# Kernel tuning notes

Hardware: AMD Instinct MI355X
Metric: run time of the kernel (lower is better)

## Reference

```python
import jax, jax.numpy as jnp
import numpy as np

NEG_INF = -1e30


def setup_inputs() -> dict:
    key = jax.random.key(0)
    kq, kk, kv, ks = jax.random.split(key, 4)
    B, H, S, D = 2, 16, 2048, 64
    return {
        "q": jax.random.normal(kq, (B, H, S, D), dtype=jnp.float32),
        "k": jax.random.normal(kk, (B, H, S, D), dtype=jnp.float32),
        "v": jax.random.normal(kv, (B, H, S, D), dtype=jnp.float32),
        "sink_weights": jax.random.normal(ks, (H,), dtype=jnp.float32),
        "sliding_window": 1024,
    }


def reference(q, k, v, sink_weights, sliding_window):
    """Sliding-window causal attention with a learnable attention-sink logit.

    Equivalent to FlexAttention.forward with sink_weights given: an extra kv
    position (the sink) is appended whose score is replaced by sink_weights[h]
    and whose value is zero -> it only adds mass to the softmax denominator.
    """
    B, H, S_q, D = q.shape
    S_kv = k.shape[2]
    scale = 1.0 / np.sqrt(D)

    # [B, H, S_q, S_kv] raw scores
    scores = jnp.einsum("bhqd,bhkd->bhqk", q, k) * scale

    q_idx = jnp.arange(S_q)[:, None]
    kv_idx = jnp.arange(S_kv)[None, :]
    keep = (kv_idx <= q_idx) & (q_idx - kv_idx <= sliding_window)  # [S_q, S_kv]
    scores = jnp.where(keep[None, None], scores, NEG_INF)

    # sink column: per-head learnable logit, always visible
    sink_col = jnp.broadcast_to(
        sink_weights[None, :, None, None], (B, H, S_q, 1)
    )
    logits = jnp.concatenate([scores, sink_col], axis=-1)  # [B,H,S_q,S_kv+1]

    probs = jax.nn.softmax(logits, axis=-1)
    # sink value is zero, so only the first S_kv prob columns hit v
    out = jnp.einsum("bhqk,bhkd->bhqd", probs[..., :S_kv], v)
    return out
```

## Files before the change

kernel.cpp:

```cpp
#include <hip/hip_runtime.h>


typedef __bf16 bf16x8 __attribute__((ext_vector_type(8)));
typedef __bf16 bf16x4 __attribute__((ext_vector_type(4)));
typedef float  f32x16 __attribute__((ext_vector_type(16)));

#define NT 256
#define NEG_BIG (-3.0e38f)

__device__ __forceinline__ int swz(int row, int gran) {
    return row * 64 + ((gran ^ ((row >> 1) & 7)) << 3);
}

__device__ __forceinline__ bf16x4 xswap32(bf16x4 v) {
    union { bf16x4 v; int i[2]; } u;
    u.v = v;
    u.i[0] = __shfl_xor(u.i[0], 32, 64);
    u.i[1] = __shfl_xor(u.i[1], 32, 64);
    return u.v;
}

__device__ const int SEG_N[24] = {3,2,2,2,2,1,2,1, 1,1,1,1,1,1,1,1, 1,1,1,1,1,1,1,1};
__device__ const int SEG_IT[24][3] = {
  {0,1,2},{2,3,0},{3,4,0},{4,5,0},{5,6,0},{6,0,0},{6,7,0},{7,0,0},
  {8,0,0},{8,0,0},{9,0,0},{9,0,0},{10,0,0},{10,0,0},{11,0,0},{11,0,0},
  {12,0,0},{12,0,0},{13,0,0},{13,0,0},{14,0,0},{14,0,0},{15,0,0},{15,0,0}};
__device__ const int SEG_J0[24][3] = {
  {0,0,0},{3,0,0},{6,0,0},{7,0,0},{6,0,0},{3,0,0},{12,0,0},{7,0,0},
  {0,0,0},{9,0,0},{0,0,0},{9,0,0},{0,0,0},{9,0,0},{0,0,0},{9,0,0},
  {0,0,0},{9,0,0},{0,0,0},{9,0,0},{0,0,0},{9,0,0},{0,0,0},{9,0,0}};
__device__ const int SEG_J1[24][3] = {
  {2,4,3},{6,6,0},{8,7,0},{10,6,0},{12,3,0},{12,0,0},{14,7,0},{16,0,0},
  {9,0,0},{18,0,0},{9,0,0},{18,0,0},{9,0,0},{18,0,0},{9,0,0},{18,0,0},
  {9,0,0},{18,0,0},{9,0,0},{18,0,0},{9,0,0},{18,0,0},{9,0,0},{18,0,0}};
__device__ const int SEG_SX[24][3] = {
  {0,0,0},{1,0,0},{1,0,0},{1,0,0},{1,0,0},{1,0,0},{2,0,0},{1,0,0},
  {0,0,0},{1,0,0},{0,0,0},{1,0,0},{0,0,0},{1,0,0},{0,0,0},{1,0,0},
  {0,0,0},{1,0,0},{0,0,0},{1,0,0},{0,0,0},{1,0,0},{0,0,0},{1,0,0}};
__device__ const int NSEG_ITEM[16] = {1,1,2,2,2,2,3,2, 2,2,2,2,2,2,2,2};

__device__ __forceinline__ void qk_mfma(const __bf16* kb, const bf16x8 bq[4],
                                        int c, int hl, f32x16& s0, f32x16& s1) {
    #pragma unroll
    for (int ks = 0; ks < 4; ++ks) {
        bf16x8 ka0 = *(const bf16x8*)&kb[swz(c,      2 * ks + hl)];
        bf16x8 ka1 = *(const bf16x8*)&kb[swz(32 + c, 2 * ks + hl)];
        s0 = __builtin_amdgcn_mfma_f32_32x32x16_bf16(ka0, bq[ks], s0, 0, 0, 0);
        s1 = __builtin_amdgcn_mfma_f32_32x32x16_bf16(ka1, bq[ks], s1, 0, 0, 0);
    }
}

__device__ __forceinline__ void pv_mfma(const __bf16* vb, const bf16x8 bp[4],
                                        int c, int hl, f32x16& o0, f32x16& o1) {
    #pragma unroll
    for (int ks = 0; ks < 4; ++ks) {
        bf16x8 va0 = *(const bf16x8*)&vb[swz(c,      2 * ks + hl)];
        bf16x8 va1 = *(const bf16x8*)&vb[swz(32 + c, 2 * ks + hl)];
        o0 = __builtin_amdgcn_mfma_f32_32x32x16_bf16(va0, bp[ks], o0, 0, 0, 0);
        o1 = __builtin_amdgcn_mfma_f32_32x32x16_bf16(va1, bp[ks], o1, 0, 0, 0);
    }
}

__device__ __forceinline__ void mask_tile(f32x16& s0, f32x16& s1,
                                          int k0, int qi, int W, int hl) {
    #pragma unroll
    for (int rg = 0; rg < 16; ++rg) {
        const int kb2 = (rg & 3) + 8 * (rg >> 2) + 4 * hl;
        const int ki0 = k0 + kb2, ki1 = k0 + 32 + kb2;
        if (!((ki0 <= qi) && (qi - ki0 <= W))) s0[rg] = -1e30f;
        if (!((ki1 <= qi) && (qi - ki1 <= W))) s1[rg] = -1e30f;
    }
}

__device__ __forceinline__ void exch_bp(const f32x16 s0, const f32x16 s1,
                                        int hl, bf16x8 bp[4]) {
    bf16x4 qA = { (__bf16)s0[0],  (__bf16)s0[1],  (__bf16)s0[2],  (__bf16)s0[3]  };
    bf16x4 qB = { (__bf16)s0[4],  (__bf16)s0[5],  (__bf16)s0[6],  (__bf16)s0[7]  };
    bf16x4 qC = { (__bf16)s0[8],  (__bf16)s0[9],  (__bf16)s0[10], (__bf16)s0[11] };
    bf16x4 qD = { (__bf16)s0[12], (__bf16)s0[13], (__bf16)s0[14], (__bf16)s0[15] };
    bf16x4 qE = { (__bf16)s1[0],  (__bf16)s1[1],  (__bf16)s1[2],  (__bf16)s1[3]  };
    bf16x4 qF = { (__bf16)s1[4],  (__bf16)s1[5],  (__bf16)s1[6],  (__bf16)s1[7]  };
    bf16x4 qG = { (__bf16)s1[8],  (__bf16)s1[9],  (__bf16)s1[10], (__bf16)s1[11] };
    bf16x4 qH = { (__bf16)s1[12], (__bf16)s1[13], (__bf16)s1[14], (__bf16)s1[15] };
    bf16x4 r0 = xswap32(hl ? qA : qB);
    bf16x4 r1 = xswap32(hl ? qC : qD);
    bf16x4 r2 = xswap32(hl ? qE : qF);
    bf16x4 r3 = xswap32(hl ? qG : qH);
    bf16x4 lo0 = hl ? r0 : qA, hi0 = hl ? qB : r0;
    bf16x4 lo1 = hl ? r1 : qC, hi1 = hl ? qD : r1;
    bf16x4 lo2 = hl ? r2 : qE, hi2 = hl ? qF : r2;
    bf16x4 lo3 = hl ? r3 : qG, hi3 = hl ? qH : r3;
    #pragma unroll
    for (int e = 0; e < 4; ++e) {
        bp[0][e] = lo0[e]; bp[0][4+e] = hi0[e];
        bp[1][e] = lo1[e]; bp[1][4+e] = hi1[e];
        bp[2][e] = lo2[e]; bp[2][4+e] = hi2[e];
        bp[3][e] = lo3[e]; bp[3][4+e] = hi3[e];
    }
}

__device__ __forceinline__ void stage_k(__bf16* dst, const float4* kr, int t) {
    #pragma unroll
    for (int i = 0; i < 4; ++i) {
        const int flat = i * NT + t;
        const int key = flat >> 4, dd = flat & 15;
        float4 f = kr[i];
        bf16x4 b = { (__bf16)f.x, (__bf16)f.y, (__bf16)f.z, (__bf16)f.w };
        *(bf16x4*)&dst[swz(key, dd >> 1) + (dd & 1) * 4] = b;
    }
}

__device__ __forceinline__ void stage_v(__bf16* dst, const float4* vr, int dgi, int kgi) {
    float4 a0 = vr[0], a1 = vr[1], a2 = vr[2], a3 = vr[3];
    bf16x4 w0 = { (__bf16)a0.x, (__bf16)a1.x, (__bf16)a2.x, (__bf16)a3.x };
    bf16x4 w1 = { (__bf16)a0.y, (__bf16)a1.y, (__bf16)a2.y, (__bf16)a3.y };
    bf16x4 w2 = { (__bf16)a0.z, (__bf16)a1.z, (__bf16)a2.z, (__bf16)a3.z };
    bf16x4 w3 = { (__bf16)a0.w, (__bf16)a1.w, (__bf16)a2.w, (__bf16)a3.w };
    const int gv = kgi >> 1, ov = (kgi & 1) * 4;
    *(bf16x4*)&dst[swz(4 * dgi + 0, gv) + ov] = w0;
    *(bf16x4*)&dst[swz(4 * dgi + 1, gv) + ov] = w1;
    *(bf16x4*)&dst[swz(4 * dgi + 2, gv) + ov] = w2;
    *(bf16x4*)&dst[swz(4 * dgi + 3, gv) + ov] = w3;
}

__global__ __launch_bounds__(NT, 2) void flex_r14_main(
    const float* __restrict__ Q, const float* __restrict__ K,
    const float* __restrict__ V, const float* __restrict__ SINKW,
    const int* __restrict__ SWIN, void* __restrict__ WS,
    float* __restrict__ OUT, const int H, const int S)
{
    const int t    = threadIdx.x;
    const int lane = t & 63;
    const int w    = t >> 6;
    const int c    = lane & 31;
    const int hl   = lane >> 5;
    const int W    = SWIN[0];
    const float scale = 0.125f;

    const int NBH = gridDim.x / 24;
    int bh, b24;
    if ((NBH & 7) == 0) {
        const int xcd  = blockIdx.x & 7;
        const int rest = blockIdx.x >> 3;
        const int G    = NBH >> 3;
        bh  = (rest % G) * 8 + xcd;
        b24 = rest / G;
    } else {
        bh  = blockIdx.x / 24;
        b24 = blockIdx.x - bh * 24;
    }
    const int h   = bh % H;
    const float sw = SINKW[h];

    __shared__ __align__(16) __bf16 k_lds[2][2][64 * 64];
    __shared__ __align__(16) __bf16 v_lds[2][2][64 * 64];

    const size_t basebh = (size_t)bh * S * 64;
    const float4* kp4 = (const float4*)(K + basebh);
    const float4* vp4 = (const float4*)(V + basebh);
    __bf16* O_ws  = (__bf16*)WS;
    float2* ml_ws = (float2*)((char*)WS + (size_t)NBH * 48 * 16384);

    const int dgi = t & 15;
    const int kgi = t >> 4;
    float4 kreg[8], vreg[8];

    const int ns = SEG_N[b24];

    {
        const int it0 = SEG_IT[b24][0];
        const int ktA0 = (2 * it0 - 16 > 0) ? (2 * it0 - 16) : 0;
        const int kt0 = ktA0 + SEG_J0[b24][0];
        #pragma unroll
        for (int i = 0; i < 4; ++i) {
            kreg[i]     = kp4[kt0 * 1024 + i * NT + t];
            kreg[4 + i] = kp4[(kt0 + 1) * 1024 + i * NT + t];
        }
        #pragma unroll
        for (int kk = 0; kk < 4; ++kk) {
            vreg[kk]     = vp4[kt0 * 1024 + (4 * kgi + kk) * 16 + dgi];
            vreg[4 + kk] = vp4[(kt0 + 1) * 1024 + (4 * kgi + kk) * 16 + dgi];
        }
        stage_k(&k_lds[0][0][0], &kreg[0], t);
        stage_v(&v_lds[0][0][0], &vreg[0], dgi, kgi);
        stage_k(&k_lds[0][1][0], &kreg[4], t);
        stage_v(&v_lds[0][1][0], &vreg[4], dgi, kgi);
    }

    int par = 0;

    for (int s = 0; s < ns; ++s) {
        const int item = SEG_IT[b24][s];
        const int j0   = SEG_J0[b24][s];
        const int j1   = SEG_J1[b24][s];
        const int sidx = SEG_SX[b24][s];
        const int ktA  = (2 * item - 16 > 0) ? (2 * item - 16) : 0;
        const int qw0  = item * 128 + 32 * w;
        const int qi   = qw0 + c;

        bf16x8 bq[4];
        {
            const float4* qp4 = (const float4*)(Q + basebh + (size_t)qi * 64);
            #pragma unroll
            for (int ks = 0; ks < 4; ++ks) {
                float4 f0 = qp4[4 * ks + 2 * hl];
                float4 f1 = qp4[4 * ks + 2 * hl + 1];
                bq[ks][0] = (__bf16)(f0.x * scale); bq[ks][1] = (__bf16)(f0.y * scale);
                bq[ks][2] = (__bf16)(f0.z * scale); bq[ks][3] = (__bf16)(f0.w * scale);
                bq[ks][4] = (__bf16)(f1.x * scale); bq[ks][5] = (__bf16)(f1.y * scale);
                bq[ks][6] = (__bf16)(f1.z * scale); bq[ks][7] = (__bf16)(f1.w * scale);
            }
        }

        float mrun = (sidx == 0) ? sw : NEG_BIG;
        float lrun = (sidx == 0) ? 1.0f : 0.0f;
        f32x16 accO0, accO1;
        #pragma unroll
        for (int i = 0; i < 16; ++i) { accO0[i] = 0.0f; accO1[i] = 0.0f; }

        for (int j = j0; j < j1; j += 2) {
            const bool two = (j + 1 < j1);
            const int k0a = (ktA + j) * 64;
            const int k0b = k0a + 64;

            __syncthreads();

            int n0 = -1, n1 = -1;
            if (j + 2 < j1) {
                n0 = ktA + j + 2;
                if (j + 3 < j1) n1 = n0 + 1;
            } else if (s + 1 < ns) {
                const int it2  = SEG_IT[b24][s + 1];
                const int ktA2 = (2 * it2 - 16 > 0) ? (2 * it2 - 16) : 0;
                const int j02  = SEG_J0[b24][s + 1];
                n0 = ktA2 + j02;
                if (j02 + 1 < SEG_J1[b24][s + 1]) n1 = n0 + 1;
            }
            if (n0 >= 0) {
                #pragma unroll
                for (int i = 0; i < 4; ++i) kreg[i] = kp4[n0 * 1024 + i * NT + t];
                #pragma unroll
                for (int kk = 0; kk < 4; ++kk) vreg[kk] = vp4[n0 * 1024 + (4 * kgi + kk) * 16 + dgi];
            }
            if (n1 >= 0) {
                #pragma unroll
                for (int i = 0; i < 4; ++i) kreg[4 + i] = kp4[n1 * 1024 + i * NT + t];
                #pragma unroll
                for (int kk = 0; kk < 4; ++kk) vreg[4 + kk] = vp4[n1 * 1024 + (4 * kgi + kk) * 16 + dgi];
            }

            f32x16 sa0, sa1, sb0, sb1;
            #pragma unroll
            for (int i = 0; i < 16; ++i) { sa0[i] = 0.0f; sa1[i] = 0.0f; sb0[i] = 0.0f; sb1[i] = 0.0f; }
            __builtin_amdgcn_s_setprio(1);
            qk_mfma(&k_lds[par][0][0], bq, c, hl, sa0, sa1);
            if (two) qk_mfma(&k_lds[par][1][0], bq, c, hl, sb0, sb1);
            __builtin_amdgcn_s_setprio(0);

            if (!((k0a + 63 <= qw0) && (qw0 + 31 - k0a <= W)))
                mask_tile(sa0, sa1, k0a, qi, W, hl);
            if (two && !((k0b + 63 <= qw0) && (qw0 + 31 - k0b <= W)))
                mask_tile(sb0, sb1, k0b, qi, W, hl);

            float m8[8];
            #pragma unroll
            for (int i = 0; i < 4; ++i) {
                m8[i]   = fmaxf(fmaxf(sa0[4*i], sa0[4*i+1]), fmaxf(sa0[4*i+2], sa0[4*i+3]));
                m8[4+i] = fmaxf(fmaxf(sa1[4*i], sa1[4*i+1]), fmaxf(sa1[4*i+2], sa1[4*i+3]));
            }
            float mx = fmaxf(fmaxf(fmaxf(m8[0], m8[1]), fmaxf(m8[2], m8[3])),
                             fmaxf(fmaxf(m8[4], m8[5]), fmaxf(m8[6], m8[7])));
            if (two) {
                float n8[8];
                #pragma unroll
                for (int i = 0; i < 4; ++i) {
                    n8[i]   = fmaxf(fmaxf(sb0[4*i], sb0[4*i+1]), fmaxf(sb0[4*i+2], sb0[4*i+3]));
                    n8[4+i] = fmaxf(fmaxf(sb1[4*i], sb1[4*i+1]), fmaxf(sb1[4*i+2], sb1[4*i+3]));
                }
                mx = fmaxf(mx, fmaxf(fmaxf(fmaxf(n8[0], n8[1]), fmaxf(n8[2], n8[3])),
                                     fmaxf(fmaxf(n8[4], n8[5]), fmaxf(n8[6], n8[7]))));
            }
            mx = fmaxf(mx, __shfl_xor(mx, 32, 64));
            if (!__all(mx <= mrun + 8.0f)) {
                const float mnew  = fmaxf(mrun, mx);
                const float alpha = __expf(mrun - mnew);
                lrun *= alpha;
                #pragma unroll
                for (int i = 0; i < 16; ++i) { accO0[i] *= alpha; accO1[i] *= alpha; }
                mrun = mnew;
            }
            float sc[8];
            #pragma unroll
            for (int i = 0; i < 8; ++i) sc[i] = 0.0f;
            #pragma unroll
            for (int i = 0; i < 16; ++i) {
                float p0 = __expf(sa0[i] - mrun); sa0[i] = p0; sc[i & 3]       += p0;
                float p1 = __expf(sa1[i] - mrun); sa1[i] = p1; sc[4 + (i & 3)] += p1;
            }
            if (two) {
                #pragma unroll
                for (int i = 0; i < 16; ++i) {
                    float p0 = __expf(sb0[i] - mrun); sb0[i] = p0; sc[i & 3]       += p0;
                    float p1 = __expf(sb1[i] - mrun); sb1[i] = p1; sc[4 + (i & 3)] += p1;
                }
            }
            float ps = ((sc[0] + sc[1]) + (sc[2] + sc[3])) + ((sc[4] + sc[5]) + (sc[6] + sc[7]));
            ps += __shfl_xor(ps, 32, 64);
            lrun += ps;

            {
                bf16x8 bp[4];
                exch_bp(sa0, sa1, hl, bp);
                __builtin_amdgcn_s_setprio(1);
                pv_mfma(&v_lds[par][0][0], bp, c, hl, accO0, accO1);
                __builtin_amdgcn_s_setprio(0);
            }
            if (two) {
                bf16x8 bp[4];
                exch_bp(sb0, sb1, hl, bp);
                __builtin_amdgcn_s_setprio(1);
                pv_mfma(&v_lds[par][1][0], bp, c, hl, accO0, accO1);
                __builtin_amdgcn_s_setprio(0);
            }

            if (n0 >= 0) {
                stage_k(&k_lds[par ^ 1][0][0], &kreg[0], t);
                stage_v(&v_lds[par ^ 1][0][0], &vreg[0], dgi, kgi);
            }
            if (n1 >= 0) {
                stage_k(&k_lds[par ^ 1][1][0], &kreg[4], t);
                stage_v(&v_lds[par ^ 1][1][0], &vreg[4], dgi, kgi);
            }
            par ^= 1;
        }

        if (item < 2) {
            const float inv = 1.0f / lrun;
            float* ob = OUT + basebh + (size_t)qi * 64;
            #pragma unroll
            for (int rg = 0; rg < 4; ++rg) {
                float4 f0 = { accO0[4*rg+0]*inv, accO0[4*rg+1]*inv,
                              accO0[4*rg+2]*inv, accO0[4*rg+3]*inv };
                float4 f1 = { accO1[4*rg+0]*inv, accO1[4*rg+1]*inv,
                              accO1[4*rg+2]*inv, accO1[4*rg+3]*inv };
                *(float4*)&ob[     8 * rg + 4 * hl] = f0;
                *(float4*)&ob[32 + 8 * rg + 4 * hl] = f1;
            }
        } else {
            const int slot = (bh * 16 + item) * 3 + sidx;
            const int qrel = 32 * w + c;
            if (hl == 0) ml_ws[(size_t)slot * 128 + qrel] = make_float2(mrun, lrun);
            __bf16* Os = O_ws + (size_t)slot * 8192 + (size_t)qrel * 64;
            #pragma unroll
            for (int qd = 0; qd < 4; ++qd) {
                const int d0 = 8 * qd + 4 * hl;
                bf16x4 b0 = { (__bf16)accO0[4*qd+0], (__bf16)accO0[4*qd+1],
                              (__bf16)accO0[4*qd+2], (__bf16)accO0[4*qd+3] };
                bf16x4 b1 = { (__bf16)accO1[4*qd+0], (__bf16)accO1[4*qd+1],
                              (__bf16)accO1[4*qd+2], (__bf16)accO1[4*qd+3] };
                *(bf16x4*)&Os[d0]      = b0;
                *(bf16x4*)&Os[32 + d0] = b1;
            }
        }
    }
}

__global__ __launch_bounds__(256) void flex_r14_combine(
    const void* __restrict__ WS, float* __restrict__ OUT, const int H, const int S)
{
    const int NBH  = gridDim.x / 14;
    const int bi   = blockIdx.x;
    const int bh   = bi / 14;
    const int item = 2 + (bi - bh * 14);
    const int ns   = NSEG_ITEM[item];
    const int t    = threadIdx.x;
    const int q    = t >> 1;
    const int half = t & 1;

    const __bf16* O_ws = (const __bf16*)WS;
    const float2* ml_ws = (const float2*)((const char*)WS + (size_t)NBH * 48 * 16384);
    const int base = (bh * 16 + item) * 3;

    float m[3], lv[3], a[3];
    float mst = NEG_BIG;
    for (int s = 0; s < ns; ++s) {
        float2 e = ml_ws[(size_t)(base + s) * 128 + q];
        m[s] = e.x; lv[s] = e.y;
        mst = fmaxf(mst, m[s]);
    }
    float lst = 0.0f;
    for (int s = 0; s < ns; ++s) { a[s] = __expf(m[s] - mst); lst += a[s] * lv[s]; }
    const float inv = 1.0f / lst;

    float acc[32];
    #pragma unroll
    for (int i = 0; i < 32; ++i) acc[i] = 0.0f;
    for (int s = 0; s < ns; ++s) {
        const __bf16* Os = O_ws + (size_t)(base + s) * 8192 + (size_t)q * 64 + 32 * half;
        const float as = a[s];
        #pragma unroll
        for (int v8 = 0; v8 < 4; ++v8) {
            bf16x8 o = *(const bf16x8*)&Os[8 * v8];
            #pragma unroll
            for (int jj = 0; jj < 8; ++jj) acc[8 * v8 + jj] += as * (float)o[jj];
        }
    }

    float* dst = OUT + (size_t)bh * S * 64 + (size_t)(item * 128 + q) * 64 + 32 * half;
    #pragma unroll
    for (int v4 = 0; v4 < 8; ++v4) {
        float4 f = { acc[4*v4+0] * inv, acc[4*v4+1] * inv,
                     acc[4*v4+2] * inv, acc[4*v4+3] * inv };
        *(float4*)&dst[4 * v4] = f;
    }
}

extern "C" void kernel_launch(void* const* d_in, const int* in_sizes, int n_in,
                              void* d_out, int out_size, void* d_ws, size_t ws_size,
                              hipStream_t stream) {
    const float* q     = (const float*)d_in[0];
    const float* k     = (const float*)d_in[1];
    const float* v     = (const float*)d_in[2];
    const float* sinkw = (const float*)d_in[3];
    const int*   swin  = (const int*)d_in[4];
    float* out = (float*)d_out;

    const int H = in_sizes[3];
    const int S = 2048;
    const int B = in_sizes[0] / (H * S * 64);
    const int NBH = B * H;

    flex_r14_main<<<dim3(NBH * 24), NT, 0, stream>>>(q, k, v, sinkw, swin, d_ws, out, H, S);
    flex_r14_combine<<<dim3(NBH * 14), 256, 0, stream>>>(d_ws, out, H, S);
}
```

Baseline: 143.5 us.

## Single-buffer K/V LDS, raise occupancy to 3, use permlane32 swaps

Replaces the double-buffered K/V shared-memory tiles with a single buffer, so each iteration stages from registers into LDS between two barriers. The prefetch global loads now move to after the softmax and before the PV MFMAs. Launch bounds rise from 2 to 3 blocks per CU, which the halved LDS footprint allows. Cross-half lane exchanges (max, sum, P operand reshuffle) switch from shfl_xor to v_permlane32_swap, dropping the hl-dependent selects. The trade-off is an extra barrier per iteration and less overlap between staging and compute, in exchange for more resident waves and cheaper exchanges.

```diff
diff --git a/kernel.cpp b/kernel.cpp
--- a/kernel.cpp
+++ b/kernel.cpp
@@ -12,12 +12,115 @@
     return row * 64 + ((gran ^ ((row >> 1) & 7)) << 3);
 }
 
-__device__ __forceinline__ bf16x4 xswap32(bf16x4 v) {
-    union { bf16x4 v; int i[2]; } u;
-    u.v = v;
-    u.i[0] = __shfl_xor(u.i[0], 32, 64);
-    u.i[1] = __shfl_xor(u.i[1], 32, 64);
-    return u.v;
+__device__ __forceinline__ void plswap(unsigned &a, unsigned &b) {
+    asm("v_permlane32_swap_b32 %0, %1" : "+v"(a), "+v"(b));
+}
+
+__device__ __forceinline__ float xmax32(float x) {
+    float a = x, b;
+    asm("v_mov_b32 %0, %1" : "=&v"(b) : "v"(a));
+    asm("v_permlane32_swap_b32 %0, %1" : "+v"(a), "+v"(b));
+    return fmaxf(a, b);
+}
+
+__device__ __forceinline__ float xsum32(float x) {
+    float a = x, b;
+    asm("v_mov_b32 %0, %1" : "=&v"(b) : "v"(a));
+    asm("v_permlane32_swap_b32 %0, %1" : "+v"(a), "+v"(b));
+    return a + b;
+}
+
+__device__ __forceinline__ void exch_bp(const f32x16& sa, const f32x16& sb,
+                                        bf16x8 bp[4]) {
+    union B4U { bf16x4 v; unsigned u[2]; };
+    B4U a0, b0, a1, b1, a2, b2, a3, b3;
+    a0.v = bf16x4{ (__bf16)sa[0],  (__bf16)sa[1],  (__bf16)sa[2],  (__bf16)sa[3]  };
+    b0.v = bf16x4{ (__bf16)sa[4],  (__bf16)sa[5],  (__bf16)sa[6],  (__bf16)sa[7]  };
+    a1.v = bf16x4{ (__bf16)sa[8],  (__bf16)sa[9],  (__bf16)sa[10], (__bf16)sa[11] };
+    b1.v = bf16x4{ (__bf16)sa[12], (__bf16)sa[13], (__bf16)sa[14], (__bf16)sa[15] };
+    a2.v = bf16x4{ (__bf16)sb[0],  (__bf16)sb[1],  (__bf16)sb[2],  (__bf16)sb[3]  };
+    b2.v = bf16x4{ (__bf16)sb[4],  (__bf16)sb[5],  (__bf16)sb[6],  (__bf16)sb[7]  };
+    a3.v = bf16x4{ (__bf16)sb[8],  (__bf16)sb[9],  (__bf16)sb[10], (__bf16)sb[11] };
+    b3.v = bf16x4{ (__bf16)sb[12], (__bf16)sb[13], (__bf16)sb[14], (__bf16)sb[15] };
+    plswap(a0.u[0], b0.u[0]); plswap(a0.u[1], b0.u[1]);
+    plswap(a1.u[0], b1.u[0]); plswap(a1.u[1], b1.u[1]);
+    plswap(a2.u[0], b2.u[0]); plswap(a2.u[1], b2.u[1]);
+    plswap(a3.u[0], b3.u[0]); plswap(a3.u[1], b3.u[1]);
+    #pragma unroll
+    for (int e = 0; e < 4; ++e) {
+        bp[0][e] = a0.v[e]; bp[0][4+e] = b0.v[e];
+        bp[1][e] = a1.v[e]; bp[1][4+e] = b1.v[e];
+        bp[2][e] = a2.v[e]; bp[2][4+e] = b2.v[e];
+        bp[3][e] = a3.v[e]; bp[3][4+e] = b3.v[e];
+    }
+}
+
+__device__ __forceinline__ void mask_tile(f32x16& s0, f32x16& s1,
+                                          int k0, int qi, int W, int hl) {
+    #pragma unroll
+    for (int rg = 0; rg < 16; ++rg) {
+        const int kb2 = (rg & 3) + 8 * (rg >> 2) + 4 * hl;
+        const int ki0 = k0 + kb2, ki1 = k0 + 32 + kb2;
+        if (!((ki0 <= qi) && (qi - ki0 <= W))) s0[rg] = -1e30f;
+        if (!((ki1 <= qi) && (qi - ki1 <= W))) s1[rg] = -1e30f;
+    }
+}
+
+__device__ __forceinline__ float tree_max(const f32x16& s0, const f32x16& s1) {
+    float q4[8];
+    #pragma unroll
+    for (int i = 0; i < 4; ++i) {
+        q4[i]   = fmaxf(fmaxf(s0[4*i], s0[4*i+1]), fmaxf(s0[4*i+2], s0[4*i+3]));
+        q4[4+i] = fmaxf(fmaxf(s1[4*i], s1[4*i+1]), fmaxf(s1[4*i+2], s1[4*i+3]));
+    }
+    return fmaxf(fmaxf(fmaxf(q4[0], q4[1]), fmaxf(q4[2], q4[3])),
+                 fmaxf(fmaxf(q4[4], q4[5]), fmaxf(q4[6], q4[7])));
+}
+
+__device__ __forceinline__ void qk_mfma(const __bf16* kb, const bf16x8 bq[4],
+                                        int c, int hl, f32x16& s0, f32x16& s1) {
+    #pragma unroll
+    for (int ks = 0; ks < 4; ++ks) {
+        bf16x8 ka0 = *(const bf16x8*)&kb[swz(c,      2 * ks + hl)];
+        bf16x8 ka1 = *(const bf16x8*)&kb[swz(32 + c, 2 * ks + hl)];
+        s0 = __builtin_amdgcn_mfma_f32_32x32x16_bf16(ka0, bq[ks], s0, 0, 0, 0);
+        s1 = __builtin_amdgcn_mfma_f32_32x32x16_bf16(ka1, bq[ks], s1, 0, 0, 0);
+    }
+}
+
+__device__ __forceinline__ void pv_mfma(const __bf16* vb, const bf16x8 bp[4],
+                                        int c, int hl, f32x16& o0, f32x16& o1) {
+    #pragma unroll
+    for (int ks = 0; ks < 4; ++ks) {
+        bf16x8 va0 = *(const bf16x8*)&vb[swz(c,      2 * ks + hl)];
+        bf16x8 va1 = *(const bf16x8*)&vb[swz(32 + c, 2 * ks + hl)];
+        o0 = __builtin_amdgcn_mfma_f32_32x32x16_bf16(va0, bp[ks], o0, 0, 0, 0);
+        o1 = __builtin_amdgcn_mfma_f32_32x32x16_bf16(va1, bp[ks], o1, 0, 0, 0);
+    }
+}
+
+__device__ __forceinline__ void stage_k(__bf16* dst, const float4* kr, int t) {
+    #pragma unroll
+    for (int i = 0; i < 4; ++i) {
+        const int flat = i * NT + t;
+        const int key = flat >> 4, dd = flat & 15;
+        float4 f = kr[i];
+        bf16x4 b = { (__bf16)f.x, (__bf16)f.y, (__bf16)f.z, (__bf16)f.w };
+        *(bf16x4*)&dst[swz(key, dd >> 1) + (dd & 1) * 4] = b;
+    }
+}
+
+__device__ __forceinline__ void stage_v(__bf16* dst, const float4* vr, int dgi, int kgi) {
+    float4 a0 = vr[0], a1 = vr[1], a2 = vr[2], a3 = vr[3];
+    bf16x4 w0 = { (__bf16)a0.x, (__bf16)a1.x, (__bf16)a2.x, (__bf16)a3.x };
+    bf16x4 w1 = { (__bf16)a0.y, (__bf16)a1.y, (__bf16)a2.y, (__bf16)a3.y };
+    bf16x4 w2 = { (__bf16)a0.z, (__bf16)a1.z, (__bf16)a2.z, (__bf16)a3.z };
+    bf16x4 w3 = { (__bf16)a0.w, (__bf16)a1.w, (__bf16)a2.w, (__bf16)a3.w };
+    const int gv = kgi >> 1, ov = (kgi & 1) * 4;
+    *(bf16x4*)&dst[swz(4 * dgi + 0, gv) + ov] = w0;
+    *(bf16x4*)&dst[swz(4 * dgi + 1, gv) + ov] = w1;
+    *(bf16x4*)&dst[swz(4 * dgi + 2, gv) + ov] = w2;
+    *(bf16x4*)&dst[swz(4 * dgi + 3, gv) + ov] = w3;
 }
 
 __device__ const int SEG_N[24] = {3,2,2,2,2,1,2,1, 1,1,1,1,1,1,1,1, 1,1,1,1,1,1,1,1};
@@ -39,91 +142,7 @@
   {0,0,0},{1,0,0},{0,0,0},{1,0,0},{0,0,0},{1,0,0},{0,0,0},{1,0,0}};
 __device__ const int NSEG_ITEM[16] = {1,1,2,2,2,2,3,2, 2,2,2,2,2,2,2,2};
 
-__device__ __forceinline__ void qk_mfma(const __bf16* kb, const bf16x8 bq[4],
-                                        int c, int hl, f32x16& s0, f32x16& s1) {
-    #pragma unroll
-    for (int ks = 0; ks < 4; ++ks) {
-        bf16x8 ka0 = *(const bf16x8*)&kb[swz(c,      2 * ks + hl)];
-        bf16x8 ka1 = *(const bf16x8*)&kb[swz(32 + c, 2 * ks + hl)];
-        s0 = __builtin_amdgcn_mfma_f32_32x32x16_bf16(ka0, bq[ks], s0, 0, 0, 0);
-        s1 = __builtin_amdgcn_mfma_f32_32x32x16_bf16(ka1, bq[ks], s1, 0, 0, 0);
-    }
-}
-
-__device__ __forceinline__ void pv_mfma(const __bf16* vb, const bf16x8 bp[4],
-                                        int c, int hl, f32x16& o0, f32x16& o1) {
-    #pragma unroll
-    for (int ks = 0; ks < 4; ++ks) {
-        bf16x8 va0 = *(const bf16x8*)&vb[swz(c,      2 * ks + hl)];
-        bf16x8 va1 = *(const bf16x8*)&vb[swz(32 + c, 2 * ks + hl)];
-        o0 = __builtin_amdgcn_mfma_f32_32x32x16_bf16(va0, bp[ks], o0, 0, 0, 0);
-        o1 = __builtin_amdgcn_mfma_f32_32x32x16_bf16(va1, bp[ks], o1, 0, 0, 0);
-    }
-}
-
-__device__ __forceinline__ void mask_tile(f32x16& s0, f32x16& s1,
-                                          int k0, int qi, int W, int hl) {
-    #pragma unroll
-    for (int rg = 0; rg < 16; ++rg) {
-        const int kb2 = (rg & 3) + 8 * (rg >> 2) + 4 * hl;
-        const int ki0 = k0 + kb2, ki1 = k0 + 32 + kb2;
-        if (!((ki0 <= qi) && (qi - ki0 <= W))) s0[rg] = -1e30f;
-        if (!((ki1 <= qi) && (qi - ki1 <= W))) s1[rg] = -1e30f;
-    }
-}
-
-__device__ __forceinline__ void exch_bp(const f32x16 s0, const f32x16 s1,
-                                        int hl, bf16x8 bp[4]) {
-    bf16x4 qA = { (__bf16)s0[0],  (__bf16)s0[1],  (__bf16)s0[2],  (__bf16)s0[3]  };
-    bf16x4 qB = { (__bf16)s0[4],  (__bf16)s0[5],  (__bf16)s0[6],  (__bf16)s0[7]  };
-    bf16x4 qC = { (__bf16)s0[8],  (__bf16)s0[9],  (__bf16)s0[10], (__bf16)s0[11] };
-    bf16x4 qD = { (__bf16)s0[12], (__bf16)s0[13], (__bf16)s0[14], (__bf16)s0[15] };
-    bf16x4 qE = { (__bf16)s1[0],  (__bf16)s1[1],  (__bf16)s1[2],  (__bf16)s1[3]  };
-    bf16x4 qF = { (__bf16)s1[4],  (__bf16)s1[5],  (__bf16)s1[6],  (__bf16)s1[7]  };
-    bf16x4 qG = { (__bf16)s1[8],  (__bf16)s1[9],  (__bf16)s1[10], (__bf16)s1[11] };
-    bf16x4 qH = { (__bf16)s1[12], (__bf16)s1[13], (__bf16)s1[14], (__bf16)s1[15] };
-    bf16x4 r0 = xswap32(hl ? qA : qB);
-    bf16x4 r1 = xswap32(hl ? qC : qD);
-    bf16x4 r2 = xswap32(hl ? qE : qF);
-    bf16x4 r3 = xswap32(hl ? qG : qH);
-    bf16x4 lo0 = hl ? r0 : qA, hi0 = hl ? qB : r0;
-    bf16x4 lo1 = hl ? r1 : qC, hi1 = hl ? qD : r1;
-    bf16x4 lo2 = hl ? r2 : qE, hi2 = hl ? qF : r2;
-    bf16x4 lo3 = hl ? r3 : qG, hi3 = hl ? qH : r3;
-    #pragma unroll
-    for (int e = 0; e < 4; ++e) {
-        bp[0][e] = lo0[e]; bp[0][4+e] = hi0[e];
-        bp[1][e] = lo1[e]; bp[1][4+e] = hi1[e];
-        bp[2][e] = lo2[e]; bp[2][4+e] = hi2[e];
-        bp[3][e] = lo3[e]; bp[3][4+e] = hi3[e];
-    }
-}
-
-__device__ __forceinline__ void stage_k(__bf16* dst, const float4* kr, int t) {
-    #pragma unroll
-    for (int i = 0; i < 4; ++i) {
-        const int flat = i * NT + t;
-        const int key = flat >> 4, dd = flat & 15;
-        float4 f = kr[i];
-        bf16x4 b = { (__bf16)f.x, (__bf16)f.y, (__bf16)f.z, (__bf16)f.w };
-        *(bf16x4*)&dst[swz(key, dd >> 1) + (dd & 1) * 4] = b;
-    }
-}
-
-__device__ __forceinline__ void stage_v(__bf16* dst, const float4* vr, int dgi, int kgi) {
-    float4 a0 = vr[0], a1 = vr[1], a2 = vr[2], a3 = vr[3];
-    bf16x4 w0 = { (__bf16)a0.x, (__bf16)a1.x, (__bf16)a2.x, (__bf16)a3.x };
-    bf16x4 w1 = { (__bf16)a0.y, (__bf16)a1.y, (__bf16)a2.y, (__bf16)a3.y };
-    bf16x4 w2 = { (__bf16)a0.z, (__bf16)a1.z, (__bf16)a2.z, (__bf16)a3.z };
-    bf16x4 w3 = { (__bf16)a0.w, (__bf16)a1.w, (__bf16)a2.w, (__bf16)a3.w };
-    const int gv = kgi >> 1, ov = (kgi & 1) * 4;
-    *(bf16x4*)&dst[swz(4 * dgi + 0, gv) + ov] = w0;
-    *(bf16x4*)&dst[swz(4 * dgi + 1, gv) + ov] = w1;
-    *(bf16x4*)&dst[swz(4 * dgi + 2, gv) + ov] = w2;
-    *(bf16x4*)&dst[swz(4 * dgi + 3, gv) + ov] = w3;
-}
-
-__global__ __launch_bounds__(NT, 2) void flex_r14_main(
+__global__ __launch_bounds__(NT, 3) void flex_r19_main(
     const float* __restrict__ Q, const float* __restrict__ K,
     const float* __restrict__ V, const float* __restrict__ SINKW,
     const int* __restrict__ SWIN, void* __restrict__ WS,
@@ -152,8 +171,8 @@
     const int h   = bh % H;
     const float sw = SINKW[h];
 
-    __shared__ __align__(16) __bf16 k_lds[2][2][64 * 64];
-    __shared__ __align__(16) __bf16 v_lds[2][2][64 * 64];
+    __shared__ __align__(16) __bf16 k_lds[2][64 * 64];
+    __shared__ __align__(16) __bf16 v_lds[2][64 * 64];
 
     const size_t basebh = (size_t)bh * S * 64;
     const float4* kp4 = (const float4*)(K + basebh);
@@ -181,13 +200,7 @@
             vreg[kk]     = vp4[kt0 * 1024 + (4 * kgi + kk) * 16 + dgi];
             vreg[4 + kk] = vp4[(kt0 + 1) * 1024 + (4 * kgi + kk) * 16 + dgi];
         }
-        stage_k(&k_lds[0][0][0], &kreg[0], t);
-        stage_v(&v_lds[0][0][0], &vreg[0], dgi, kgi);
-        stage_k(&k_lds[0][1][0], &kreg[4], t);
-        stage_v(&v_lds[0][1][0], &vreg[4], dgi, kgi);
-    }
-
-    int par = 0;
+    }
 
     for (int s = 0; s < ns; ++s) {
         const int item = SEG_IT[b24][s];
@@ -222,6 +235,15 @@
             const bool two = (j + 1 < j1);
             const int k0a = (ktA + j) * 64;
             const int k0b = k0a + 64;
+
+            __syncthreads();
+
+            stage_k(&k_lds[0][0], &kreg[0], t);
+            stage_v(&v_lds[0][0], &vreg[0], dgi, kgi);
+            if (two) {
+                stage_k(&k_lds[1][0], &kreg[4], t);
+                stage_v(&v_lds[1][0], &vreg[4], dgi, kgi);
+            }
 
             __syncthreads();
 
@@ -236,25 +258,13 @@
                 n0 = ktA2 + j02;
                 if (j02 + 1 < SEG_J1[b24][s + 1]) n1 = n0 + 1;
             }
-            if (n0 >= 0) {
-                #pragma unroll
-                for (int i = 0; i < 4; ++i) kreg[i] = kp4[n0 * 1024 + i * NT + t];
-                #pragma unroll
-                for (int kk = 0; kk < 4; ++kk) vreg[kk] = vp4[n0 * 1024 + (4 * kgi + kk) * 16 + dgi];
-            }
-            if (n1 >= 0) {
-                #pragma unroll
-                for (int i = 0; i < 4; ++i) kreg[4 + i] = kp4[n1 * 1024 + i * NT + t];
-                #pragma unroll
-                for (int kk = 0; kk < 4; ++kk) vreg[4 + kk] = vp4[n1 * 1024 + (4 * kgi + kk) * 16 + dgi];
-            }
 
             f32x16 sa0, sa1, sb0, sb1;
             #pragma unroll
             for (int i = 0; i < 16; ++i) { sa0[i] = 0.0f; sa1[i] = 0.0f; sb0[i] = 0.0f; sb1[i] = 0.0f; }
             __builtin_amdgcn_s_setprio(1);
-            qk_mfma(&k_lds[par][0][0], bq, c, hl, sa0, sa1);
-            if (two) qk_mfma(&k_lds[par][1][0], bq, c, hl, sb0, sb1);
+            qk_mfma(&k_lds[0][0], bq, c, hl, sa0, sa1);
+            if (two) qk_mfma(&k_lds[1][0], bq, c, hl, sb0, sb1);
             __builtin_amdgcn_s_setprio(0);
 
             if (!((k0a + 63 <= qw0) && (qw0 + 31 - k0a <= W)))
@@ -262,25 +272,9 @@
             if (two && !((k0b + 63 <= qw0) && (qw0 + 31 - k0b <= W)))
                 mask_tile(sb0, sb1, k0b, qi, W, hl);
 
-            float m8[8];
-            #pragma unroll
-            for (int i = 0; i < 4; ++i) {
-                m8[i]   = fmaxf(fmaxf(sa0[4*i], sa0[4*i+1]), fmaxf(sa0[4*i+2], sa0[4*i+3]));
-                m8[4+i] = fmaxf(fmaxf(sa1[4*i], sa1[4*i+1]), fmaxf(sa1[4*i+2], sa1[4*i+3]));
-            }
-            float mx = fmaxf(fmaxf(fmaxf(m8[0], m8[1]), fmaxf(m8[2], m8[3])),
-                             fmaxf(fmaxf(m8[4], m8[5]), fmaxf(m8[6], m8[7])));
-            if (two) {
-                float n8[8];
-                #pragma unroll
-                for (int i = 0; i < 4; ++i) {
-                    n8[i]   = fmaxf(fmaxf(sb0[4*i], sb0[4*i+1]), fmaxf(sb0[4*i+2], sb0[4*i+3]));
-                    n8[4+i] = fmaxf(fmaxf(sb1[4*i], sb1[4*i+1]), fmaxf(sb1[4*i+2], sb1[4*i+3]));
-                }
-                mx = fmaxf(mx, fmaxf(fmaxf(fmaxf(n8[0], n8[1]), fmaxf(n8[2], n8[3])),
-                                     fmaxf(fmaxf(n8[4], n8[5]), fmaxf(n8[6], n8[7]))));
-            }
-            mx = fmaxf(mx, __shfl_xor(mx, 32, 64));
+            float mx = tree_max(sa0, sa1);
+            if (two) mx = fmaxf(mx, tree_max(sb0, sb1));
+            mx = xmax32(mx);
             if (!__all(mx <= mrun + 8.0f)) {
                 const float mnew  = fmaxf(mrun, mx);
                 const float alpha = __expf(mrun - mnew);
@@ -305,33 +299,29 @@
                 }
             }
             float ps = ((sc[0] + sc[1]) + (sc[2] + sc[3])) + ((sc[4] + sc[5]) + (sc[6] + sc[7]));
-            ps += __shfl_xor(ps, 32, 64);
-            lrun += ps;
-
-            {
-                bf16x8 bp[4];
-                exch_bp(sa0, sa1, hl, bp);
-                __builtin_amdgcn_s_setprio(1);
-                pv_mfma(&v_lds[par][0][0], bp, c, hl, accO0, accO1);
-                __builtin_amdgcn_s_setprio(0);
-            }
-            if (two) {
-                bf16x8 bp[4];
-                exch_bp(sb0, sb1, hl, bp);
-                __builtin_amdgcn_s_setprio(1);
-                pv_mfma(&v_lds[par][1][0], bp, c, hl, accO0, accO1);
-                __builtin_amdgcn_s_setprio(0);
-            }
+            lrun += xsum32(ps);
+
+            bf16x8 bpa[4], bpb[4];
+            exch_bp(sa0, sa1, bpa);
+            if (two) exch_bp(sb0, sb1, bpb);
 
             if (n0 >= 0) {
-                stage_k(&k_lds[par ^ 1][0][0], &kreg[0], t);
-                stage_v(&v_lds[par ^ 1][0][0], &vreg[0], dgi, kgi);
+                #pragma unroll
+                for (int i = 0; i < 4; ++i) kreg[i] = kp4[n0 * 1024 + i * NT + t];
+                #pragma unroll
+                for (int kk = 0; kk < 4; ++kk) vreg[kk] = vp4[n0 * 1024 + (4 * kgi + kk) * 16 + dgi];
             }
             if (n1 >= 0) {
-                stage_k(&k_lds[par ^ 1][1][0], &kreg[4], t);
-                stage_v(&v_lds[par ^ 1][1][0], &vreg[4], dgi, kgi);
-            }
-            par ^= 1;
+                #pragma unroll
+                for (int i = 0; i < 4; ++i) kreg[4 + i] = kp4[n1 * 1024 + i * NT + t];
+                #pragma unroll
+                for (int kk = 0; kk < 4; ++kk) vreg[4 + kk] = vp4[n1 * 1024 + (4 * kgi + kk) * 16 + dgi];
+            }
+
+            __builtin_amdgcn_s_setprio(1);
+            pv_mfma(&v_lds[0][0], bpa, c, hl, accO0, accO1);
+            if (two) pv_mfma(&v_lds[1][0], bpb, c, hl, accO0, accO1);
+            __builtin_amdgcn_s_setprio(0);
         }
 
         if (item < 2) {
@@ -365,7 +355,7 @@
     }
 }
 
-__global__ __launch_bounds__(256) void flex_r14_combine(
+__global__ __launch_bounds__(256) void flex_r19_combine(
     const void* __restrict__ WS, float* __restrict__ OUT, const int H, const int S)
 {
     const int NBH  = gridDim.x / 14;
@@ -430,6 +420,6 @@
     const int B = in_sizes[0] / (H * S * 64);
     const int NBH = B * H;
 
-    flex_r14_main<<<dim3(NBH * 24), NT, 0, stream>>>(q, k, v, sinkw, swin, d_ws, out, H, S);
-    flex_r14_combine<<<dim3(NBH * 14), 256, 0, stream>>>(d_ws, out, H, S);
-}
+    flex_r19_main<<<dim3(NBH * 24), NT, 0, stream>>>(q, k, v, sinkw, swin, d_ws, out, H, S);
+    flex_r19_combine<<<dim3(NBH * 14), 256, 0, stream>>>(d_ws, out, H, S);
+}
```

Measured after the change: 236.2 us. 1.65x slower.
